# Kernel optimization log

Measured on AMD Instinct MI355X. Metric: run time of the kernel, lower is better.

The kernel has to match this reference:

```python
import jax, jax.numpy as jnp
import numpy as np

B, S, D = 2, 2048, 1024
H = 16
HD = D // H  # 64
THETA = 10000.0


def apply_rope(x, positions, theta):
    # x: (b, h, s, hd); positions: (s,)
    hd = x.shape[-1]
    inv_freq = theta ** (-jnp.arange(0, hd, 2, dtype=jnp.float32) / hd)  # (hd/2,)
    angles = positions.astype(jnp.float32)[:, None] * inv_freq[None, :]  # (s, hd/2)
    cos, sin = jnp.cos(angles), jnp.sin(angles)
    x1 = x[..., 0::2]
    x2 = x[..., 1::2]
    r1 = x1 * cos - x2 * sin
    r2 = x1 * sin + x2 * cos
    out = jnp.stack([r1, r2], axis=-1).reshape(x.shape)
    return out.astype(x.dtype)


def setup_inputs() -> dict:
    key = jax.random.key(0)
    ks = jax.random.split(key, 5)
    scale = 1.0 / np.sqrt(D)
    return {
        "in_features": jax.random.normal(ks[0], (B, S, D), dtype=jnp.float32),
        "token_positions": jnp.arange(S, dtype=jnp.int32),
        "Wq": jax.random.normal(ks[1], (D, D), dtype=jnp.float32) * scale,
        "Wk": jax.random.normal(ks[2], (D, D), dtype=jnp.float32) * scale,
        "Wv": jax.random.normal(ks[3], (D, D), dtype=jnp.float32) * scale,
        "Wo": jax.random.normal(ks[4], (D, D), dtype=jnp.float32) * scale,
    }


def reference(in_features, token_positions, Wq, Wk, Wv, Wo):
    b, s, d = in_features.shape
    h, hd = H, HD
    # bias-free linear: y = x @ W.T  (W is (out, in))
    q = in_features @ Wq.T
    k = in_features @ Wk.T
    v = in_features @ Wv.T
    # (b, s, h*hd) -> (b, h, s, hd)
    split = lambda t: t.reshape(b, s, h, hd).transpose(0, 2, 1, 3)
    q, k, v = split(q), split(k), split(v)
    q = apply_rope(q, token_positions, THETA)
    k = apply_rope(k, token_positions, THETA)
    scores = jnp.einsum("bhid,bhjd->bhij", q, k) / jnp.sqrt(jnp.asarray(hd, dtype=q.dtype))
    causal = jnp.triu(jnp.ones((s, s), dtype=bool), k=1)
    scores = jnp.where(causal, -jnp.inf, scores)
    attn = jax.nn.softmax(scores, axis=-1)
    out = jnp.einsum("bhij,bhjd->bhid", attn, v)
    out = out.transpose(0, 2, 1, 3).reshape(b, s, d)
    return out @ Wo.T
```

## Files before the change

kernel.cpp:

```cpp
#include <hip/hip_runtime.h>
#include <math.h>

#define NUM_HEADS 16
#define HEAD_DIM 64

typedef __bf16 bf16x8 __attribute__((ext_vector_type(8)));
typedef short shortx4 __attribute__((ext_vector_type(4)));
typedef float floatx4 __attribute__((ext_vector_type(4)));

#if __has_builtin(__builtin_amdgcn_exp2f)
#define EXP2(x) __builtin_amdgcn_exp2f(x)
#else
#define EXP2(x) exp2f(x)
#endif

__device__ __forceinline__ unsigned short f2b(float f) {
  unsigned int u = __float_as_uint(f);
  u += 0x7fffu + ((u >> 16) & 1u);
  return (unsigned short)(u >> 16);
}

__device__ __forceinline__ void async16(const void* g, void* l) {
  __builtin_amdgcn_global_load_lds(
      (const __attribute__((address_space(1))) unsigned int*)g,
      (__attribute__((address_space(3))) unsigned int*)l, 16, 0, 0);
}

__device__ __forceinline__ void cvt4(const float* in, unsigned short* out, int i) {
  float4 v = ((const float4*)in)[i];
  ushort4 o;
  o.x = f2b(v.x); o.y = f2b(v.y); o.z = f2b(v.z); o.w = f2b(v.w);
  ((ushort4*)out)[i] = o;
}

__global__ void prep(const float* __restrict__ x,
                     const float* __restrict__ w0, const float* __restrict__ w1,
                     const float* __restrict__ w2, const float* __restrict__ w3,
                     const int* __restrict__ pos,
                     unsigned short* Xb, unsigned short* o0, unsigned short* o1,
                     unsigned short* o2, unsigned short* o3,
                     float* __restrict__ tab, int xq, int w4, int ntab) {
  int i = blockIdx.x * 256 + threadIdx.x;
  int z = blockIdx.y;
  if (z == 0) {
    if (i < xq) {
#pragma unroll
      for (int rep = 0; rep < 4; ++rep) cvt4(x, Xb, rep * xq + i);
    }
  } else if (z <= 4) {
    if (i < w4) {
      const float* in = (z == 1) ? w0 : (z == 2) ? w1 : (z == 3) ? w2 : w3;
      unsigned short* out = (z == 1) ? o0 : (z == 2) ? o1 : (z == 3) ? o2 : o3;
      cvt4(in, out, i);
    }
  } else {
    if (i < ntab) {
      int fi = i & 31, s = i >> 5;
      float inv = expf(-0.28782313662425575f * (float)fi);
      float ang = (float)pos[s] * inv;
      float sn, cs;
      sincosf(ang, &sn, &cs);
      tab[i * 2] = cs;
      tab[i * 2 + 1] = sn;
    }
  }
}

template <int MODE, int MT>
__global__ __launch_bounds__(256, MODE == 1 ? 4 : 2)
void gemm_bt(const unsigned short* __restrict__ A,
             const unsigned short* __restrict__ B0,
             const unsigned short* __restrict__ B1,
             const unsigned short* __restrict__ B2,
             void* out0v, void* out1v, void* out2v,
             const float* __restrict__ ctab,
             int M, int N, int K, int S) {
  __shared__ unsigned short As[(MT / 16) * 512];
  __shared__ unsigned short Bs[8 * 512];
  const int tid = threadIdx.x;
  const int lane = tid & 63;
  const int w = tid >> 6;
  const int lane16 = lane & 15;
  const int g = lane >> 4;
  const int wm = w >> 1, wn = w & 1;
  const int m0 = blockIdx.y * MT;
  const int n0 = blockIdx.x * 128;
  const unsigned short* Bp = (blockIdx.z == 0) ? B0 : (blockIdx.z == 1 ? B1 : B2);
  constexpr int MTILES = MT / 32;

  const floatx4 vzero = {0.f, 0.f, 0.f, 0.f};
  floatx4 acc[MTILES][4];
#pragma unroll
  for (int i = 0; i < MTILES; i++)
#pragma unroll
    for (int j = 0; j < 4; j++) acc[i][j] = vzero;

  const int ar = lane >> 2;
  const int ac = (lane & 3) * 8;

  for (int k0 = 0; k0 < K; k0 += 32) {
    if constexpr (MT == 128) {
#pragma unroll
      for (int c = 0; c < 2; c++) {
        int chunk = w * 2 + c;
        async16(A  + (size_t)(m0 + chunk * 16 + ar) * K + k0 + ac, As + chunk * 512);
        async16(Bp + (size_t)(n0 + chunk * 16 + ar) * K + k0 + ac, Bs + chunk * 512);
      }
    } else {
      async16(A  + (size_t)(m0 + w * 16 + ar) * K + k0 + ac, As + w * 512);
      async16(Bp + (size_t)(n0 + w * 16 + ar) * K + k0 + ac, Bs + w * 512);
      async16(Bp + (size_t)(n0 + (w + 4) * 16 + ar) * K + k0 + ac, Bs + (w + 4) * 512);
    }
    __syncthreads();
    bf16x8 a[MTILES], b[4];
#pragma unroll
    for (int mt = 0; mt < MTILES; mt++)
      a[mt] = *(const bf16x8*)&As[(wm * (MT / 2) + mt * 16 + lane16) * 32 + g * 8];
#pragma unroll
    for (int nt = 0; nt < 4; nt++)
      b[nt] = *(const bf16x8*)&Bs[(wn * 64 + nt * 16 + lane16) * 32 + g * 8];
#pragma unroll
    for (int mt = 0; mt < MTILES; mt++)
#pragma unroll
      for (int nt = 0; nt < 4; nt++)
        acc[mt][nt] = __builtin_amdgcn_mfma_f32_16x16x32_bf16(b[nt], a[mt], acc[mt][nt], 0, 0, 0);
    __syncthreads();
  }

  if (MODE == 0) {
    if (blockIdx.z < 2) {
      unsigned short* outp = (unsigned short*)((blockIdx.z == 0) ? out0v : out1v);
      const float qs = (blockIdx.z == 0) ? 0.18033688011112042f : 1.0f;
#pragma unroll
      for (int mt = 0; mt < MTILES; mt++) {
        int m = m0 + wm * (MT / 2) + mt * 16 + lane16;
        int bb = m / S, s = m - bb * S;
        const float* crow = ctab + (size_t)s * 64;
#pragma unroll
        for (int nt = 0; nt < 4; nt++) {
          int n = n0 + wn * 64 + nt * 16 + g * 4;
          int h = n >> 6, dl = n & 63;
          floatx4 v = acc[mt][nt];
          float4 cs = *(const float4*)&crow[dl];
          float r0 = (v[0] * cs.x - v[1] * cs.y) * qs;
          float r1 = (v[0] * cs.y + v[1] * cs.x) * qs;
          float r2 = (v[2] * cs.z - v[3] * cs.w) * qs;
          float r3 = (v[2] * cs.w + v[3] * cs.z) * qs;
          shortx4 st;
          st[0] = (short)f2b(r0); st[1] = (short)f2b(r1);
          st[2] = (short)f2b(r2); st[3] = (short)f2b(r3);
          *(shortx4*)&outp[(((size_t)(bb * NUM_HEADS + h) * S + s) << 6) + dl] = st;
        }
      }
    } else {
      unsigned short* outp = (unsigned short*)out2v;
#pragma unroll
      for (int mt = 0; mt < MTILES; mt++) {
        int m = m0 + wm * (MT / 2) + mt * 16 + lane16;
        int bb = m / S, s = m - bb * S;
#pragma unroll
        for (int nt = 0; nt < 4; nt++) {
          int n = n0 + wn * 64 + nt * 16 + g * 4;
          int bh = bb * NUM_HEADS + (n >> 6);
          int dl = n & 63;
          size_t dbase = ((size_t)bh * 64 + dl) * S + s;
#pragma unroll
          for (int r = 0; r < 4; r++)
            outp[dbase + (size_t)r * S] = f2b(acc[mt][nt][r]);
        }
      }
    }
  } else {
    float* outp = (float*)out0v;
#pragma unroll
    for (int mt = 0; mt < MTILES; mt++) {
      int m = m0 + wm * (MT / 2) + mt * 16 + lane16;
#pragma unroll
      for (int nt = 0; nt < 4; nt++) {
        int n = n0 + wn * 64 + nt * 16 + g * 4;
        *(floatx4*)&outp[(size_t)m * N + n] = acc[mt][nt];
      }
    }
  }
}

__global__ __launch_bounds__(256, 2)
void flash_attn5(const unsigned short* __restrict__ Q,
                 const unsigned short* __restrict__ Kv,
                 const unsigned short* __restrict__ Vt,
                 unsigned short* __restrict__ Oattn, int S) {
  __shared__ unsigned short Ks[2 * 4096];
  __shared__ unsigned short Vs[2 * 4096];
  const int tid = threadIdx.x;
  const int lane = tid & 63;
  const int w = tid >> 6;
  const int lane16 = lane & 15;
  const int g = lane >> 4;
  const int sw = lane16 & 7;
  const int NT = S >> 6;
  const int qa = blockIdx.x;
  const int qb = NT - 1 - qa;
  const int bh = blockIdx.y;
  const int b = bh >> 4, h = bh & 15;
  const size_t kbase = (size_t)bh * S * HEAD_DIM;
  const unsigned short* Kbase = Kv + kbase;
  const unsigned short* Vtbase = Vt + (size_t)bh * HEAD_DIM * S;
  const int qrowA = qa * 64 + w * 16;
  const int qrowB = qb * 64 + w * 16;

  bf16x8 qA0, qA1, qB0, qB1;
  {
    const unsigned short* qp = Q + kbase + (size_t)(qrowA + lane16) * HEAD_DIM + g * 8;
    qA0 = *(const bf16x8*)qp;
    qA1 = *(const bf16x8*)(qp + 32);
    qp = Q + kbase + (size_t)(qrowB + lane16) * HEAD_DIM + g * 8;
    qB0 = *(const bf16x8*)qp;
    qB1 = *(const bf16x8*)(qp + 32);
  }

  const int ci0 = w * 64 + lane;
  const int ci1 = ci0 + 256;
  const int r0 = ci0 >> 3, j0 = (ci0 & 7) ^ (r0 & 7);
  const int r1 = ci1 >> 3, j1 = (ci1 & 7) ^ (r1 & 7);
  const unsigned short* kS0 = Kbase + r0 * HEAD_DIM + j0 * 8;
  const unsigned short* kS1 = Kbase + r1 * HEAD_DIM + j1 * 8;
  const unsigned short* vS0 = Vtbase + (size_t)r0 * S + j0 * 8;
  const unsigned short* vS1 = Vtbase + (size_t)r1 * S + j1 * 8;
  unsigned short* kD0 = Ks + ci0 * 8;
  unsigned short* kD1 = Ks + ci1 * 8;
  unsigned short* vD0 = Vs + ci0 * 8;
  unsigned short* vD1 = Vs + ci1 * 8;

  auto stage = [&](int t, int bi) {
    int koff = t * 4096;
    int voff = t * 64;
    int doff = bi * 4096;
    async16(kS0 + koff, kD0 + doff);
    async16(kS1 + koff, kD1 + doff);
    async16(vS0 + voff, vD0 + doff);
    async16(vS1 + voff, vD1 + doff);
  };

  const floatx4 vzero = {0.f, 0.f, 0.f, 0.f};
  floatx4 oA[4], oB[4];
#pragma unroll
  for (int i = 0; i < 4; i++) { oA[i] = vzero; oB[i] = vzero; }
  float lA = 0.f, lB = 0.f;

  stage(0, 0);
  __syncthreads();

  for (int t = 0; t <= qb; ++t) {
    const int bi = t & 1;
    if (t < qb) stage(t + 1, bi ^ 1);
    const unsigned short* Kb_ = Ks + bi * 4096;
    const unsigned short* Vb_ = Vs + bi * 4096;
    const bool doA = (t <= qa);

    bf16x8 kf0[4], kf1[4];
#pragma unroll
    for (int c = 0; c < 4; ++c) {
      int r = c * 16 + lane16;
      kf0[c] = *(const bf16x8*)&Kb_[(r * 8 + (g ^ sw)) * 8];
      kf1[c] = *(const bf16x8*)&Kb_[(r * 8 + ((4 + g) ^ sw)) * 8];
    }

    floatx4 scB[4];
#pragma unroll
    for (int c = 0; c < 4; ++c) {
      floatx4 s = vzero;
      s = __builtin_amdgcn_mfma_f32_16x16x32_bf16(kf0[c], qB0, s, 0, 0, 0);
      s = __builtin_amdgcn_mfma_f32_16x16x32_bf16(kf1[c], qB1, s, 0, 0, 0);
      scB[c] = s;
    }
    if (t == qb) {
      const int i = qrowB + lane16;
      const int jb = t * 64;
#pragma unroll
      for (int c = 0; c < 4; ++c)
#pragma unroll
        for (int r = 0; r < 4; ++r)
          if (jb + c * 16 + g * 4 + r > i) scB[c][r] = -INFINITY;
    }
    shortx4 pcB[4], pcA[4];
#pragma unroll
    for (int c = 0; c < 4; ++c) {
      float p0 = EXP2(scB[c][0]);
      float p1 = EXP2(scB[c][1]);
      float p2 = EXP2(scB[c][2]);
      float p3 = EXP2(scB[c][3]);
      lB += (p0 + p1) + (p2 + p3);
      union { unsigned int u[2]; shortx4 s4; } pu;
      pu.u[0] = __builtin_amdgcn_perm(__float_as_uint(p1), __float_as_uint(p0), 0x07060302u);
      pu.u[1] = __builtin_amdgcn_perm(__float_as_uint(p3), __float_as_uint(p2), 0x07060302u);
      pcB[c] = pu.s4;
    }

    if (doA) {
      floatx4 scA[4];
#pragma unroll
      for (int c = 0; c < 4; ++c) {
        floatx4 s = vzero;
        s = __builtin_amdgcn_mfma_f32_16x16x32_bf16(kf0[c], qA0, s, 0, 0, 0);
        s = __builtin_amdgcn_mfma_f32_16x16x32_bf16(kf1[c], qA1, s, 0, 0, 0);
        scA[c] = s;
      }
      if (t == qa) {
        const int i = qrowA + lane16;
        const int jb = t * 64;
#pragma unroll
        for (int c = 0; c < 4; ++c)
#pragma unroll
          for (int r = 0; r < 4; ++r)
            if (jb + c * 16 + g * 4 + r > i) scA[c][r] = -INFINITY;
      }
#pragma unroll
      for (int c = 0; c < 4; ++c) {
        float p0 = EXP2(scA[c][0]);
        float p1 = EXP2(scA[c][1]);
        float p2 = EXP2(scA[c][2]);
        float p3 = EXP2(scA[c][3]);
        lA += (p0 + p1) + (p2 + p3);
        union { unsigned int u[2]; shortx4 s4; } pu;
        pu.u[0] = __builtin_amdgcn_perm(__float_as_uint(p1), __float_as_uint(p0), 0x07060302u);
        pu.u[1] = __builtin_amdgcn_perm(__float_as_uint(p3), __float_as_uint(p2), 0x07060302u);
        pcA[c] = pu.s4;
      }
#pragma unroll
      for (int nt = 0; nt < 4; ++nt) {
        int rv = nt * 16 + lane16;
#pragma unroll
        for (int c = 0; c < 4; ++c) {
          shortx4 vf = *(const shortx4*)&Vb_[(rv * 8 + ((c * 2 + (g >> 1)) ^ sw)) * 8 + (g & 1) * 4];
          oB[nt] = __builtin_amdgcn_mfma_f32_16x16x16bf16_1k(vf, pcB[c], oB[nt], 0, 0, 0);
          oA[nt] = __builtin_amdgcn_mfma_f32_16x16x16bf16_1k(vf, pcA[c], oA[nt], 0, 0, 0);
        }
      }
    } else {
#pragma unroll
      for (int nt = 0; nt < 4; ++nt) {
        int rv = nt * 16 + lane16;
#pragma unroll
        for (int c = 0; c < 4; ++c) {
          shortx4 vf = *(const shortx4*)&Vb_[(rv * 8 + ((c * 2 + (g >> 1)) ^ sw)) * 8 + (g & 1) * 4];
          oB[nt] = __builtin_amdgcn_mfma_f32_16x16x16bf16_1k(vf, pcB[c], oB[nt], 0, 0, 0);
        }
      }
    }
    __syncthreads();
  }

  {
    float l = lA;
    l += __shfl_xor(l, 16, 64);
    l += __shfl_xor(l, 32, 64);
    float inv = 1.0f / l;
    int srow = qrowA + lane16;
    size_t rowb = ((size_t)b * S + srow) * 1024 + h * 64;
#pragma unroll
    for (int nt = 0; nt < 4; ++nt) {
      shortx4 st;
#pragma unroll
      for (int r = 0; r < 4; ++r) st[r] = (short)f2b(oA[nt][r] * inv);
      *(shortx4*)&Oattn[rowb + nt * 16 + g * 4] = st;
    }
  }
  {
    float l = lB;
    l += __shfl_xor(l, 16, 64);
    l += __shfl_xor(l, 32, 64);
    float inv = 1.0f / l;
    int srow = qrowB + lane16;
    size_t rowb = ((size_t)b * S + srow) * 1024 + h * 64;
#pragma unroll
    for (int nt = 0; nt < 4; ++nt) {
      shortx4 st;
#pragma unroll
      for (int r = 0; r < 4; ++r) st[r] = (short)f2b(oB[nt][r] * inv);
      *(shortx4*)&Oattn[rowb + nt * 16 + g * 4] = st;
    }
  }
}

extern "C" void kernel_launch(void* const* d_in, const int* in_sizes, int n_in,
                              void* d_out, int out_size, void* d_ws, size_t ws_size,
                              hipStream_t stream) {
  const float* x  = (const float*)d_in[0];
  const int*  pos = (const int*)d_in[1];
  const float* wq = (const float*)d_in[2];
  const float* wk = (const float*)d_in[3];
  const float* wv = (const float*)d_in[4];
  const float* wo = (const float*)d_in[5];

  const int D = 1024;
  const int S = in_sizes[1];
  const int M = in_sizes[0] / D;
  const int B = M / S;
  const int BH = B * NUM_HEADS;

  char* wsb = (char*)d_ws;
  size_t off = 0;
  auto alloc = [&](size_t bytes) {
    char* p = wsb + off;
    off += (bytes + 255) & ~(size_t)255;
    return p;
  };
  unsigned short* Xb   = (unsigned short*)alloc((size_t)M * D * 2);
  unsigned short* Wqb  = (unsigned short*)alloc((size_t)D * D * 2);
  unsigned short* Wkb  = (unsigned short*)alloc((size_t)D * D * 2);
  unsigned short* Wvb  = (unsigned short*)alloc((size_t)D * D * 2);
  unsigned short* Wob  = (unsigned short*)alloc((size_t)D * D * 2);
  unsigned short* Qb   = (unsigned short*)alloc((size_t)M * D * 2);
  unsigned short* Kb   = (unsigned short*)alloc((size_t)M * D * 2);
  unsigned short* Vtb  = (unsigned short*)alloc((size_t)M * D * 2);
  unsigned short* Attn = (unsigned short*)alloc((size_t)M * D * 2);
  float*          Ctab = (float*)alloc((size_t)S * 32 * 2 * 4);
  (void)ws_size;

  {
    int n4x = M * D / 4;
    int xq = n4x / 4;
    int w4 = D * D / 4;
    int ntab = S * 32;
    int gx = (w4 + 255) / 256;
    prep<<<dim3(gx, 6), 256, 0, stream>>>(x, wq, wk, wv, wo, pos,
                                          Xb, Wqb, Wkb, Wvb, Wob, Ctab,
                                          xq, w4, ntab);
  }
  gemm_bt<0, 128><<<dim3(D / 128, M / 128, 3), 256, 0, stream>>>(
      Xb, Wqb, Wkb, Wvb, Qb, Kb, Vtb, Ctab, M, D, D, S);
  flash_attn5<<<dim3(S / 128, BH), 256, 0, stream>>>(Qb, Kb, Vtb, Attn, S);
  gemm_bt<1, 64><<<dim3(D / 128, M / 64, 1), 256, 0, stream>>>(
      Attn, Wob, Wob, Wob, d_out, d_out, d_out, Ctab, M, D, D, S);
}
```

Baseline: 181.0 us.

## Deepen flash-attention K/V prefetch to four buffers and remap blocks per XCD

Expands the K/V shared-memory ring from two to four buffers and keeps up to three tiles of async global-to-LDS loads in flight, using explicit vmcnt waits and a single barrier per iteration instead of two. Also remaps the block index so all query tiles of a given batch-head land on the same XCD, improving L2 reuse of K/V. The cost is doubled LDS use per block (which may limit occupancy) and fragile hand-written waitcnt logic.

Measured after the change: 178.8 us. Within noise of the previous version (-1.2%).

```diff
diff --git a/kernel.cpp b/kernel.cpp
--- a/kernel.cpp
+++ b/kernel.cpp
@@ -185,12 +185,12 @@
 }
 
 __global__ __launch_bounds__(256, 2)
-void flash_attn5(const unsigned short* __restrict__ Q,
+void flash_attn7(const unsigned short* __restrict__ Q,
                  const unsigned short* __restrict__ Kv,
                  const unsigned short* __restrict__ Vt,
                  unsigned short* __restrict__ Oattn, int S) {
-  __shared__ unsigned short Ks[2 * 4096];
-  __shared__ unsigned short Vs[2 * 4096];
+  __shared__ unsigned short Ks[4 * 4096];
+  __shared__ unsigned short Vs[4 * 4096];
   const int tid = threadIdx.x;
   const int lane = tid & 63;
   const int w = tid >> 6;
@@ -198,9 +198,21 @@
   const int g = lane >> 4;
   const int sw = lane16 & 7;
   const int NT = S >> 6;
-  const int qa = blockIdx.x;
+  int qa, bh;
+  {
+    int nx = gridDim.x, ny = gridDim.y;
+    int flat = blockIdx.y * nx + blockIdx.x;
+    if ((ny & 7) == 0) {
+      int xcd = flat & 7;
+      int idx = flat >> 3;
+      int per = ny >> 3;
+      bh = xcd * per + (idx % per);
+      qa = idx / per;
+    } else {
+      qa = blockIdx.x; bh = blockIdx.y;
+    }
+  }
   const int qb = NT - 1 - qa;
-  const int bh = blockIdx.y;
   const int b = bh >> 4, h = bh & 15;
   const size_t kbase = (size_t)bh * S * HEAD_DIM;
   const unsigned short* Kbase = Kv + kbase;
@@ -248,11 +260,24 @@
   float lA = 0.f, lB = 0.f;
 
   stage(0, 0);
-  __syncthreads();
+  __builtin_amdgcn_sched_barrier(0);
+  if (qb >= 1) stage(1, 1);
+  __builtin_amdgcn_sched_barrier(0);
+  if (qb >= 2) stage(2, 2);
+  __builtin_amdgcn_sched_barrier(0);
 
   for (int t = 0; t <= qb; ++t) {
-    const int bi = t & 1;
-    if (t < qb) stage(t + 1, bi ^ 1);
+    const int bi = t & 3;
+    const int rem = qb - t;
+    if (rem >= 2)      asm volatile("s_waitcnt vmcnt(8)" ::: "memory");
+    else if (rem == 1) asm volatile("s_waitcnt vmcnt(4)" ::: "memory");
+    else               asm volatile("s_waitcnt vmcnt(0)" ::: "memory");
+    __builtin_amdgcn_sched_barrier(0);
+    __builtin_amdgcn_s_barrier();
+    __builtin_amdgcn_sched_barrier(0);
+    if (t + 3 <= qb) stage(t + 3, (t + 3) & 3);
+    __builtin_amdgcn_sched_barrier(0);
+
     const unsigned short* Kb_ = Ks + bi * 4096;
     const unsigned short* Vb_ = Vs + bi * 4096;
     const bool doA = (t <= qa);
@@ -260,9 +285,9 @@
     bf16x8 kf0[4], kf1[4];
 #pragma unroll
     for (int c = 0; c < 4; ++c) {
-      int r = c * 16 + lane16;
-      kf0[c] = *(const bf16x8*)&Kb_[(r * 8 + (g ^ sw)) * 8];
-      kf1[c] = *(const bf16x8*)&Kb_[(r * 8 + ((4 + g) ^ sw)) * 8];
+      int rr = c * 16 + lane16;
+      kf0[c] = *(const bf16x8*)&Kb_[(rr * 8 + (g ^ sw)) * 8];
+      kf1[c] = *(const bf16x8*)&Kb_[(rr * 8 + ((4 + g) ^ sw)) * 8];
     }
 
     floatx4 scB[4];
@@ -347,7 +372,6 @@
         }
       }
     }
-    __syncthreads();
   }
 
   {
@@ -429,7 +453,7 @@
   }
   gemm_bt<0, 128><<<dim3(D / 128, M / 128, 3), 256, 0, stream>>>(
       Xb, Wqb, Wkb, Wvb, Qb, Kb, Vtb, Ctab, M, D, D, S);
-  flash_attn5<<<dim3(S / 128, BH), 256, 0, stream>>>(Qb, Kb, Vtb, Attn, S);
+  flash_attn7<<<dim3(S / 128, BH), 256, 0, stream>>>(Qb, Kb, Vtb, Attn, S);
   gemm_bt<1, 64><<<dim3(D / 128, M / 64, 1), 256, 0, stream>>>(
       Attn, Wob, Wob, Wob, d_out, d_out, d_out, Ctab, M, D, D, S);
 }
```
